# Kernel tuning notes

Hardware: AMD Instinct MI355X
Metric: run time of the kernel (lower is better)

The kernel has to match this reference:

```python
import jax, jax.numpy as jnp
import numpy as np
import math

D_EMBED = 128   # per-head dim (config.d_embed)
N_HEADS = 12
ROPE_BASE = 10000.0


def rope(x):
    # x: [B, H, S, D]; interleaved-pair rotary embedding on last dim
    B, H, S, D = x.shape
    half = D // 2
    inv_freq = 1.0 / (ROPE_BASE ** (jnp.arange(0, half, dtype=jnp.float32) * 2.0 / D))
    ang = jnp.arange(S, dtype=jnp.float32)[:, None] * inv_freq[None, :]  # [S, D/2]
    cos, sin = jnp.cos(ang), jnp.sin(ang)
    xp = x.reshape(B, H, S, half, 2)
    x1, x2 = xp[..., 0], xp[..., 1]
    o1 = x1 * cos - x2 * sin
    o2 = x1 * sin + x2 * cos
    return jnp.stack([o1, o2], axis=-1).reshape(B, H, S, D)


def setup_inputs() -> dict:
    key = jax.random.key(0)
    ks = jax.random.split(key, 5)
    B, S, E = 2, 2048, D_EMBED // 2
    inner = N_HEADS * D_EMBED
    sc = 0.02
    return {
        "q": jax.random.normal(ks[0], (B, S, E), dtype=jnp.float32),
        "Wq": jax.random.normal(ks[1], (inner, E), dtype=jnp.float32) * sc,
        "Wk": jax.random.normal(ks[2], (inner, E), dtype=jnp.float32) * sc,
        "Wv": jax.random.normal(ks[3], (inner, E), dtype=jnp.float32) * sc,
        "Wo": jax.random.normal(ks[4], (E, inner), dtype=jnp.float32) * sc,
    }


def reference(q, Wq, Wk, Wv, Wo):
    B, S, E = q.shape
    H, D = N_HEADS, D_EMBED
    scale = 1.0 / math.sqrt(D)

    def proj(x, W):
        return (x @ W.T).reshape(B, S, H, D).transpose(0, 2, 1, 3)  # [B,H,S,D]

    qh = rope(proj(q, Wq))
    kh = rope(proj(q, Wk))
    vh = proj(q, Wv)

    scores = jnp.einsum("bhsd,bhtd->bhst", qh, kh) * scale  # [B,H,S,S]
    causal = jnp.tril(jnp.ones((S, S), dtype=bool))
    scores = jnp.where(causal, scores, -jnp.inf)
    probs = jax.nn.softmax(scores, axis=-1)  # dropout omitted (eval mode)
    out = jnp.einsum("bhst,bhtd->bhsd", probs, vh)
    out = out.transpose(0, 2, 1, 3).reshape(B, S, H * D)
    return out @ Wo.T  # [B,S,E]
```

## Files before the change

kernel.cpp:

```cpp
#include <hip/hip_runtime.h>
#include <stdint.h>


typedef short v8s __attribute__((ext_vector_type(8)));
typedef unsigned int v4u __attribute__((ext_vector_type(4)));
typedef float v4f __attribute__((ext_vector_type(4)));
typedef float v16f __attribute__((ext_vector_type(16)));

#define MFMA16(a, b, c) __builtin_amdgcn_mfma_f32_16x16x32_bf16(a, b, c, 0, 0, 0)
#define MFMA32(a, b, c) __builtin_amdgcn_mfma_f32_32x32x16_bf16(a, b, c, 0, 0, 0)

#if __has_builtin(__builtin_amdgcn_exp2f)
#define EXP2(x) __builtin_amdgcn_exp2f(x)
#else
#define EXP2(x) exp2f(x)
#endif

#define SCALE2 (0.08838834764831845f * 1.4426950408889634f)

__device__ __forceinline__ unsigned short f2bf(float f) {
  uint32_t u = __builtin_bit_cast(uint32_t, f);
  u += 0x7FFFu + ((u >> 16) & 1u);
  return (unsigned short)(u >> 16);
}

__device__ __forceinline__ uint32_t packbf(float lo, float hi) {
  return __builtin_amdgcn_perm(__builtin_bit_cast(uint32_t, hi) + 0x8000u,
                               __builtin_bit_cast(uint32_t, lo) + 0x8000u,
                               0x07060302u);
}

__device__ __forceinline__ v16f zero16() {
  v16f z;
#pragma unroll
  for (int i = 0; i < 16; ++i) z[i] = 0.f;
  return z;
}

__device__ __forceinline__ void gl_lds16(const unsigned short* g, unsigned short* l) {
  __builtin_amdgcn_global_load_lds(
      (const __attribute__((address_space(1))) uint32_t*)g,
      (__attribute__((address_space(3))) uint32_t*)l, 16, 0, 0);
}

__global__ __launch_bounds__(256) void rope_table(float* __restrict__ cos_t,
                                                  float* __restrict__ sin_t) {
  int idx = blockIdx.x * 256 + threadIdx.x;
  if (idx >= 2048 * 64) return;
  int s = idx >> 6, f = idx & 63;
  float inv = exp2f((float)f * -0.20762050593046014f);
  float ang = (float)s * inv;
  float si, co;
  sincosf(ang, &si, &co);
  cos_t[idx] = co;
  sin_t[idx] = si;
}

__global__ __launch_bounds__(256) void proj_rope(
    const float* __restrict__ x, const float* __restrict__ Wq,
    const float* __restrict__ Wk, const float* __restrict__ Wv,
    const float* __restrict__ cos_t, const float* __restrict__ sin_t,
    unsigned short* __restrict__ qh, unsigned short* __restrict__ kh,
    unsigned short* __restrict__ vt) {
  const int wave = threadIdx.x >> 6, lane = threadIdx.x & 63;
  const int l16 = lane & 15, quad = lane >> 4;
  const int by = blockIdx.y;
  const int o_base = by * 64 + wave * 16;
  const int mat = o_base / 1536;
  const int inner0 = o_base % 1536;
  const int d0w = inner0 & 127;
  const float* Wsrc = (mat == 0) ? Wq : ((mat == 1) ? Wk : Wv);
  const float qscale = (mat == 0) ? SCALE2 : 1.0f;

  __shared__ __align__(16) unsigned short Lt[64][72];

  v8s wb[2];
  {
    const float* wr = Wsrc + (size_t)(inner0 + l16) * 64 + quad * 8;
#pragma unroll
    for (int s = 0; s < 2; ++s) {
      float4 a = *(const float4*)(wr + s * 32);
      float4 b = *(const float4*)(wr + s * 32 + 4);
      v8s t;
      t[0] = (short)f2bf(a.x); t[1] = (short)f2bf(a.y);
      t[2] = (short)f2bf(a.z); t[3] = (short)f2bf(a.w);
      t[4] = (short)f2bf(b.x); t[5] = (short)f2bf(b.y);
      t[6] = (short)f2bf(b.z); t[7] = (short)f2bf(b.w);
      wb[s] = t;
    }
  }

  const int d = d0w + l16;
  const int half = d >> 1;

#pragma unroll
  for (int i = 0; i < 4; ++i) {
    const int tok0 = blockIdx.x * 64 + i * 16;
    const float* xr = x + (size_t)(tok0 + l16) * 64 + quad * 8;
    v8s xa[2];
#pragma unroll
    for (int s = 0; s < 2; ++s) {
      float4 a = *(const float4*)(xr + s * 32);
      float4 b = *(const float4*)(xr + s * 32 + 4);
      v8s t;
      t[0] = (short)f2bf(a.x); t[1] = (short)f2bf(a.y);
      t[2] = (short)f2bf(a.z); t[3] = (short)f2bf(a.w);
      t[4] = (short)f2bf(b.x); t[5] = (short)f2bf(b.y);
      t[6] = (short)f2bf(b.z); t[7] = (short)f2bf(b.w);
      xa[s] = t;
    }
    v4f acc = {0.f, 0.f, 0.f, 0.f};
    acc = MFMA16(xa[0], wb[0], acc);
    acc = MFMA16(xa[1], wb[1], acc);

    if (mat < 2) {
#pragma unroll
      for (int r = 0; r < 4; ++r) {
        int sidx = (tok0 + quad * 4 + r) & 2047;
        float val = acc[r];
        float prt = __shfl_xor(val, 1);
        float co = cos_t[sidx * 64 + half];
        float si = sin_t[sidx * 64 + half];
        float rot = ((d & 1) == 0) ? (val * co - prt * si)
                                   : (prt * si + val * co);
        Lt[i * 16 + quad * 4 + r][wave * 16 + l16] = f2bf(rot * qscale);
      }
    } else {
#pragma unroll
      for (int r = 0; r < 4; ++r)
        Lt[wave * 16 + l16][i * 16 + quad * 4 + r] = f2bf(acc[r]);
    }
  }
  __syncthreads();

  const int matb = (by * 64) / 1536;
  const int innerb = (by * 64) % 1536;
  const int hb = innerb >> 7;
  const int d0b = innerb & 127;
  const int b = (blockIdx.x * 64) >> 11;
  const int tokbase = (blockIdx.x * 64) & 2047;
#pragma unroll
  for (int jj = 0; jj < 2; ++jj) {
    int cid = jj * 256 + threadIdx.x;
    int outer = cid >> 3, ic = cid & 7;
    v8s val = *(const v8s*)&Lt[outer][ic * 8];
    if (matb < 2) {
      unsigned short* dst = (matb == 0 ? qh : kh) +
          (((size_t)(b * 12 + hb)) * 2048 + tokbase + outer) * 128 + d0b + ic * 8;
      *(v8s*)dst = val;
    } else {
      const int kt = tokbase >> 6;
      const int G = ic >> 1, hhb = ic & 1;
      const int dd = d0b + outer;
      unsigned short* dst = vt +
          ((((((size_t)(b * 12 + hb)) * 32 + kt) * 4 + G) * 4 + (dd >> 5)) * 64 +
           hhb * 32 + (dd & 31)) * 8;
      *(v8s*)dst = val;
    }
  }
}

__global__ __launch_bounds__(512, 2) void attn(
    const unsigned short* __restrict__ qh, const unsigned short* __restrict__ kh,
    const unsigned short* __restrict__ vtf, unsigned short* __restrict__ att,
    const float* __restrict__ Wo, unsigned short* __restrict__ wob) {
  const int bh = blockIdx.x;
  const int qb = 15 - (int)blockIdx.y;
  const int t = threadIdx.x;
  const int lane = t & 63;
  const int l31 = lane & 31, hh = lane >> 5;
  const int w = t >> 6;
  const int rg = w & 3, kherd = w >> 2;
  const int r0w = qb * 128 + rg * 32;
  const int qrow = r0w + l31;
  const int rowmax = r0w + 31;

  const unsigned short* Qb = qh + (size_t)bh * 2048 * 128;
  const unsigned short* Kb = kh + (size_t)bh * 2048 * 128;
  const unsigned short* Vb = vtf + (size_t)bh * 262144;

  __shared__ __align__(16) unsigned short KSH[4 * 8192];

  v8s qa[8];
  {
    const unsigned short* qr = Qb + (size_t)qrow * 128 + hh * 8;
#pragma unroll
    for (int ks = 0; ks < 8; ++ks) qa[ks] = *(const v8s*)(qr + ks * 16);
  }

  int offK[2];
#pragma unroll
  for (int i2 = 0; i2 < 2; ++i2) {
    int flat = i2 * 512 + t;
    int kr = flat >> 4, kc = flat & 15;
    offK[i2] = kr * 128 + ((kc ^ (kr & 15)) << 3);
  }
  auto stageT = [&](int ktile, int slot) {
    const unsigned short* kg = Kb + ((size_t)(ktile << 6)) * 128;
    unsigned short* db = &KSH[slot * 8192];
#pragma unroll
    for (int i2 = 0; i2 < 2; ++i2)
      gl_lds16(kg + offK[i2], db + ((i2 * 512 + t) << 3));
  };

  v16f O[4];
#pragma unroll
  for (int i = 0; i < 4; ++i) O[i] = zero16();
  float lsum = 0.f;

  const int NS = qb + 1;
  stageT(0, 0);
  stageT(qb + 1, 2);
  asm volatile("s_waitcnt vmcnt(0)" ::: "memory");

  for (int i = 0; i < NS; ++i) {
    __builtin_amdgcn_s_barrier();
    __builtin_amdgcn_sched_barrier(0);
    const int kt = kherd ? (qb + 1 + i) : i;
    const int key0 = kt << 6;
    const bool active = key0 <= rowmax;
    const bool hi = (key0 + 32) <= rowmax;

    v8s v0a[4], v0b[4], v1a[4], v1b[4];
    if (active) {
      const unsigned short* Vt = Vb + (size_t)kt * 8192;
#pragma unroll
      for (int dt = 0; dt < 4; ++dt)
        v0a[dt] = *(const v8s*)(Vt + ((0 * 4 + dt) * 64 + lane) * 8);
#pragma unroll
      for (int dt = 0; dt < 4; ++dt)
        v0b[dt] = *(const v8s*)(Vt + ((1 * 4 + dt) * 64 + lane) * 8);
      if (hi) {
#pragma unroll
        for (int dt = 0; dt < 4; ++dt)
          v1a[dt] = *(const v8s*)(Vt + ((2 * 4 + dt) * 64 + lane) * 8);
#pragma unroll
        for (int dt = 0; dt < 4; ++dt)
          v1b[dt] = *(const v8s*)(Vt + ((3 * 4 + dt) * 64 + lane) * 8);
      }
    }
    __builtin_amdgcn_sched_barrier(0);

    if (i + 1 < NS) {
      stageT(i + 1, (i + 1) & 1);
      stageT(qb + 2 + i, 2 + ((i + 1) & 1));
    }
    __builtin_amdgcn_sched_barrier(0);

    if (active) {
      const unsigned short* Kl = &KSH[(kherd * 2 + (i & 1)) * 8192];
      const bool mask0 = (key0 + 31) > r0w;
      const bool mask1 = (key0 + 63) > r0w;

      auto softpack = [&](const v16f& SS, const v16f& ST, int kh2, bool needmask,
                          uint32_t* W) {
#pragma unroll
        for (int m = 0; m < 8; ++m) {
          float pa = EXP2(SS[2 * m] + ST[2 * m]);
          float pb = EXP2(SS[2 * m + 1] + ST[2 * m + 1]);
          if (needmask) {
            int keyb = key0 + kh2 * 32 + 2 * (m & 1) + 8 * (m >> 1) + 4 * hh;
            pa = (keyb <= qrow) ? pa : 0.f;
            pb = (keyb + 1 <= qrow) ? pb : 0.f;
          }
          lsum += pa + pb;
          W[m] = packbf(pa, pb);
        }
      };
      auto pvhalf = [&](const uint32_t* W, int kh2, const v8s* vA, const v8s* vB) {
        uint32_t r0 = __shfl_xor(hh ? W[0] : W[2], 32);
        uint32_t r1 = __shfl_xor(hh ? W[1] : W[3], 32);
        uint32_t r2 = __shfl_xor(hh ? W[4] : W[6], 32);
        uint32_t r3 = __shfl_xor(hh ? W[5] : W[7], 32);
#pragma unroll
        for (int gl = 0; gl < 2; ++gl) {
          const int g = kh2 * 2 + gl;
          if (key0 + g * 16 > rowmax) continue;
          uint32_t rA = gl ? r2 : r0, rB = gl ? r3 : r1;
          v4u fw;
          fw.x = hh ? rA : W[4 * gl];
          fw.y = hh ? rB : W[4 * gl + 1];
          fw.z = hh ? W[4 * gl + 2] : rA;
          fw.w = hh ? W[4 * gl + 3] : rB;
          v8s pfrag = __builtin_bit_cast(v8s, fw);
          const v8s* vv = gl ? vB : vA;
          __builtin_amdgcn_s_setprio(1);
#pragma unroll
          for (int dt = 0; dt < 4; ++dt) O[dt] = MFMA32(vv[dt], pfrag, O[dt]);
          __builtin_amdgcn_s_setprio(0);
        }
      };

      v16f Sa = zero16(), Sb = zero16();
      __builtin_amdgcn_s_setprio(1);
#pragma unroll
      for (int ks = 0; ks < 8; ks += 2) {
        v8s ka0 = *(const v8s*)(
            Kl + ((l31 * 16 + ((2 * ks + hh) ^ (l31 & 15))) << 3));
        v8s ka1 = *(const v8s*)(
            Kl + ((l31 * 16 + ((2 * ks + 2 + hh) ^ (l31 & 15))) << 3));
        Sa = MFMA32(ka0, qa[ks], Sa);
        Sb = MFMA32(ka1, qa[ks + 1], Sb);
      }
      __builtin_amdgcn_s_setprio(0);
      uint32_t W0[8];
      softpack(Sa, Sb, 0, mask0, W0);
      pvhalf(W0, 0, v0a, v0b);

      if (hi) {
        v16f Sc = zero16(), Sd = zero16();
        __builtin_amdgcn_s_setprio(1);
#pragma unroll
        for (int ks = 0; ks < 8; ks += 2) {
          v8s ka0 = *(const v8s*)(
              Kl + (((32 + l31) * 16 + ((2 * ks + hh) ^ (l31 & 15))) << 3));
          v8s ka1 = *(const v8s*)(
              Kl + (((32 + l31) * 16 + ((2 * ks + 2 + hh) ^ (l31 & 15))) << 3));
          Sc = MFMA32(ka0, qa[ks], Sc);
          Sd = MFMA32(ka1, qa[ks + 1], Sd);
        }
        __builtin_amdgcn_s_setprio(0);
        uint32_t W1[8];
        softpack(Sc, Sd, 1, mask1, W1);
        pvhalf(W1, 1, v1a, v1b);
      }
    }
    asm volatile("s_waitcnt vmcnt(0)" ::: "memory");
  }

  __syncthreads();
  float* Ored = (float*)KSH;
  if (kherd == 1) {
    float* baseO = Ored + rg * 4096 + l31 * 128;
#pragma unroll
    for (int dt = 0; dt < 4; ++dt)
#pragma unroll
      for (int pr = 0; pr < 4; ++pr) {
        float4 v;
        v.x = O[dt][4 * pr + 0]; v.y = O[dt][4 * pr + 1];
        v.z = O[dt][4 * pr + 2]; v.w = O[dt][4 * pr + 3];
        *(float4*)(baseO + dt * 32 + (((2 * pr + hh) ^ (l31 & 7)) << 2)) = v;
      }
  }
  __syncthreads();
  if (kherd == 0) {
    const float* baseO = Ored + rg * 4096 + l31 * 128;
#pragma unroll
    for (int dt = 0; dt < 4; ++dt)
#pragma unroll
      for (int pr = 0; pr < 4; ++pr) {
        float4 v = *(const float4*)(
            baseO + dt * 32 + (((2 * pr + hh) ^ (l31 & 7)) << 2));
        O[dt][4 * pr + 0] += v.x;
        O[dt][4 * pr + 1] += v.y;
        O[dt][4 * pr + 2] += v.z;
        O[dt][4 * pr + 3] += v.w;
      }
  }
  __syncthreads();
  if (kherd == 1) Ored[rg * 64 + lane] = lsum;
  __syncthreads();
  if (kherd == 0) {
    const float lt = lsum + Ored[rg * 64 + lane];
    const float tot = lt + __shfl_xor(lt, 32);
    const float inv = 1.0f / tot;
    const int b = bh / 12, hq = bh % 12;
    unsigned short* arow = att + ((size_t)b * 2048 + qrow) * 1536 + hq * 128;
#pragma unroll
    for (int dt = 0; dt < 4; ++dt) {
#pragma unroll
      for (int pr = 0; pr < 4; ++pr) {
        float a0 = O[dt][4 * pr + 0] * inv;
        float a1 = O[dt][4 * pr + 1] * inv;
        float a2 = O[dt][4 * pr + 2] * inv;
        float a3 = O[dt][4 * pr + 3] * inv;
        uint2 uu;
        uu.x = packbf(a0, a1);
        uu.y = packbf(a2, a3);
        *(uint2*)(arow + dt * 32 + 8 * pr + 4 * hh) = uu;
      }
    }
  }

  if (qb == 0) {
    const int base = bh * 4096;
#pragma unroll
    for (int i = 0; i < 8; ++i)
      wob[base + i * 512 + t] = f2bf(Wo[base + i * 512 + t]);
  }
}

__global__ __launch_bounds__(256) void outproj(
    const unsigned short* __restrict__ att, const unsigned short* __restrict__ wob,
    float* __restrict__ out) {
  const int wave = threadIdx.x >> 6, lane = threadIdx.x & 63;
  const int l16 = lane & 15, quad = lane >> 4;
  const int tok0 = blockIdx.x * 16;
  const int e0 = wave * 16;

  v4f acc0 = {0.f, 0.f, 0.f, 0.f}, acc1 = {0.f, 0.f, 0.f, 0.f};
  const unsigned short* ar = att + (size_t)(tok0 + l16) * 1536 + quad * 8;
  const unsigned short* wr = wob + (size_t)(e0 + l16) * 1536 + quad * 8;
#pragma unroll 4
  for (int s = 0; s < 24; ++s) {
    v8s a0 = *(const v8s*)(ar + (2 * s) * 32);
    v8s b0 = *(const v8s*)(wr + (2 * s) * 32);
    v8s a1 = *(const v8s*)(ar + (2 * s + 1) * 32);
    v8s b1 = *(const v8s*)(wr + (2 * s + 1) * 32);
    acc0 = MFMA16(a0, b0, acc0);
    acc1 = MFMA16(a1, b1, acc1);
  }
#pragma unroll
  for (int r = 0; r < 4; ++r)
    out[(size_t)(tok0 + quad * 4 + r) * 64 + e0 + l16] = acc0[r] + acc1[r];
}

extern "C" void kernel_launch(void* const* d_in, const int* in_sizes, int n_in,
                              void* d_out, int out_size, void* d_ws,
                              size_t ws_size, hipStream_t stream) {
  const float* q  = (const float*)d_in[0];
  const float* Wq = (const float*)d_in[1];
  const float* Wk = (const float*)d_in[2];
  const float* Wv = (const float*)d_in[3];
  const float* Wo = (const float*)d_in[4];
  float* out = (float*)d_out;

  unsigned short* ws = (unsigned short*)d_ws;
  unsigned short* qh  = ws;
  unsigned short* kh  = ws + 6291456;
  unsigned short* vtf = ws + 12582912;
  unsigned short* att = ws + 18874368;
  float* cos_t = (float*)((char*)d_ws + 50331648);
  float* sin_t = cos_t + 131072;
  unsigned short* wob = (unsigned short*)cos_t;

  rope_table<<<512, 256, 0, stream>>>(cos_t, sin_t);
  proj_rope<<<dim3(64, 72), 256, 0, stream>>>(q, Wq, Wk, Wv, cos_t, sin_t,
                                              qh, kh, vtf);
  attn<<<dim3(24, 16), 512, 0, stream>>>(qh, kh, vtf, att, Wo, wob);
  outproj<<<256, 256, 0, stream>>>(att, wob, out);
}
```

Before: 184.0 us.

## Stage V tiles through LDS and reorder attention blocks heavy-first

V tiles are now copied asynchronously into a double-buffered LDS region alongside K, instead of being loaded from global memory into registers at the top of each iteration. The PV MFMAs then read their V operands from LDS. The 2D grid becomes a 1D grid with an explicit block order: heavy causal query blocks go first and mid-size ones are placed to balance the tail. The cost is 128KB of dynamic LDS per block, which likely limits each CU to one block despite launch bounds of two, and so lowers occupancy.

```diff
diff --git a/kernel.cpp b/kernel.cpp
--- a/kernel.cpp
+++ b/kernel.cpp
@@ -164,8 +164,17 @@
     const unsigned short* __restrict__ qh, const unsigned short* __restrict__ kh,
     const unsigned short* __restrict__ vtf, unsigned short* __restrict__ att,
     const float* __restrict__ Wo, unsigned short* __restrict__ wob) {
-  const int bh = blockIdx.x;
-  const int qb = 15 - (int)blockIdx.y;
+  extern __shared__ __align__(16) unsigned short SH[];
+  unsigned short* KSH = SH;
+  unsigned short* VSH = SH + 32768;
+
+  const int n = blockIdx.x;
+  int qb, bh;
+  if (n < 240)      { qb = 15 - n / 24; bh = n % 24; }
+  else if (n < 256) { qb = 5;           bh = n - 240; }
+  else if (n < 376) { int r = n - 256; qb = r / 24; bh = r % 24; }
+  else              { qb = 5;           bh = 16 + (n - 376); }
+
   const int t = threadIdx.x;
   const int lane = t & 63;
   const int l31 = lane & 31, hh = lane >> 5;
@@ -179,8 +188,6 @@
   const unsigned short* Kb = kh + (size_t)bh * 2048 * 128;
   const unsigned short* Vb = vtf + (size_t)bh * 262144;
 
-  __shared__ __align__(16) unsigned short KSH[4 * 8192];
-
   v8s qa[8];
   {
     const unsigned short* qr = Qb + (size_t)qrow * 128 + hh * 8;
@@ -195,13 +202,20 @@
     int kr = flat >> 4, kc = flat & 15;
     offK[i2] = kr * 128 + ((kc ^ (kr & 15)) << 3);
   }
-  auto stageT = [&](int ktile, int slot) {
+  auto stageK = [&](int ktile, int slot) {
     const unsigned short* kg = Kb + ((size_t)(ktile << 6)) * 128;
     unsigned short* db = &KSH[slot * 8192];
 #pragma unroll
     for (int i2 = 0; i2 < 2; ++i2)
       gl_lds16(kg + offK[i2], db + ((i2 * 512 + t) << 3));
   };
+  auto stageV = [&](int ktile, int slot) {
+    const unsigned short* vg = Vb + (size_t)ktile * 8192;
+    unsigned short* db = &VSH[slot * 8192];
+#pragma unroll
+    for (int i2 = 0; i2 < 2; ++i2)
+      gl_lds16(vg + ((i2 * 512 + t) << 3), db + ((i2 * 512 + t) << 3));
+  };
 
   v16f O[4];
 #pragma unroll
@@ -209,8 +223,8 @@
   float lsum = 0.f;
 
   const int NS = qb + 1;
-  stageT(0, 0);
-  stageT(qb + 1, 2);
+  stageK(0, 0); stageV(0, 0);
+  stageK(qb + 1, 2); stageV(qb + 1, 2);
   asm volatile("s_waitcnt vmcnt(0)" ::: "memory");
 
   for (int i = 0; i < NS; ++i) {
@@ -221,34 +235,17 @@
     const bool active = key0 <= rowmax;
     const bool hi = (key0 + 32) <= rowmax;
 
-    v8s v0a[4], v0b[4], v1a[4], v1b[4];
-    if (active) {
-      const unsigned short* Vt = Vb + (size_t)kt * 8192;
-#pragma unroll
-      for (int dt = 0; dt < 4; ++dt)
-        v0a[dt] = *(const v8s*)(Vt + ((0 * 4 + dt) * 64 + lane) * 8);
-#pragma unroll
-      for (int dt = 0; dt < 4; ++dt)
-        v0b[dt] = *(const v8s*)(Vt + ((1 * 4 + dt) * 64 + lane) * 8);
-      if (hi) {
-#pragma unroll
-        for (int dt = 0; dt < 4; ++dt)
-          v1a[dt] = *(const v8s*)(Vt + ((2 * 4 + dt) * 64 + lane) * 8);
-#pragma unroll
-        for (int dt = 0; dt < 4; ++dt)
-          v1b[dt] = *(const v8s*)(Vt + ((3 * 4 + dt) * 64 + lane) * 8);
-      }
-    }
-    __builtin_amdgcn_sched_barrier(0);
-
     if (i + 1 < NS) {
-      stageT(i + 1, (i + 1) & 1);
-      stageT(qb + 2 + i, 2 + ((i + 1) & 1));
+      stageK(i + 1, (i + 1) & 1);
+      stageV(i + 1, (i + 1) & 1);
+      stageK(qb + 2 + i, 2 + ((i + 1) & 1));
+      stageV(qb + 2 + i, 2 + ((i + 1) & 1));
     }
     __builtin_amdgcn_sched_barrier(0);
 
     if (active) {
       const unsigned short* Kl = &KSH[(kherd * 2 + (i & 1)) * 8192];
+      const unsigned short* Vl = &VSH[(kherd * 2 + (i & 1)) * 8192];
       const bool mask0 = (key0 + 31) > r0w;
       const bool mask1 = (key0 + 63) > r0w;
 
@@ -267,7 +264,7 @@
           W[m] = packbf(pa, pb);
         }
       };
-      auto pvhalf = [&](const uint32_t* W, int kh2, const v8s* vA, const v8s* vB) {
+      auto pvhalf = [&](const uint32_t* W, int kh2) {
         uint32_t r0 = __shfl_xor(hh ? W[0] : W[2], 32);
         uint32_t r1 = __shfl_xor(hh ? W[1] : W[3], 32);
         uint32_t r2 = __shfl_xor(hh ? W[4] : W[6], 32);
@@ -283,10 +280,12 @@
           fw.z = hh ? W[4 * gl + 2] : rA;
           fw.w = hh ? W[4 * gl + 3] : rB;
           v8s pfrag = __builtin_bit_cast(v8s, fw);
-          const v8s* vv = gl ? vB : vA;
           __builtin_amdgcn_s_setprio(1);
 #pragma unroll
-          for (int dt = 0; dt < 4; ++dt) O[dt] = MFMA32(vv[dt], pfrag, O[dt]);
+          for (int dt = 0; dt < 4; ++dt) {
+            v8s va = *(const v8s*)(Vl + (((g * 4 + dt) * 64 + lane) << 3));
+            O[dt] = MFMA32(va, pfrag, O[dt]);
+          }
           __builtin_amdgcn_s_setprio(0);
         }
       };
@@ -305,7 +304,7 @@
       __builtin_amdgcn_s_setprio(0);
       uint32_t W0[8];
       softpack(Sa, Sb, 0, mask0, W0);
-      pvhalf(W0, 0, v0a, v0b);
+      pvhalf(W0, 0);
 
       if (hi) {
         v16f Sc = zero16(), Sd = zero16();
@@ -322,7 +321,7 @@
         __builtin_amdgcn_s_setprio(0);
         uint32_t W1[8];
         softpack(Sc, Sd, 1, mask1, W1);
-        pvhalf(W1, 1, v1a, v1b);
+        pvhalf(W1, 1);
       }
     }
     asm volatile("s_waitcnt vmcnt(0)" ::: "memory");
@@ -434,9 +433,12 @@
   float* sin_t = cos_t + 131072;
   unsigned short* wob = (unsigned short*)cos_t;
 
+  hipFuncSetAttribute((const void*)attn,
+                      hipFuncAttributeMaxDynamicSharedMemorySize, 131072);
+
   rope_table<<<512, 256, 0, stream>>>(cos_t, sin_t);
   proj_rope<<<dim3(64, 72), 256, 0, stream>>>(q, Wq, Wk, Wv, cos_t, sin_t,
                                               qh, kh, vtf);
-  attn<<<dim3(24, 16), 512, 0, stream>>>(qh, kh, vtf, att, Wo, wob);
+  attn<<<dim3(384), 512, 131072, stream>>>(qh, kh, vtf, att, Wo, wob);
   outproj<<<256, 256, 0, stream>>>(att, wob, out);
 }
```

New measurement: 181.2 us. No clear change (-1.5%).
